# Kernel optimization log

Hardware: AMD Instinct MI355X
Metric: run time of the kernel (lower is better)

The kernel has to match this reference:

```python
import jax, jax.numpy as jnp
import numpy as np

NUMERICAL_STABILIZER = 1e-3


def relu_kernel(data, projection_matrix):
    # data: [B,L,H,D], projection_matrix: [M,D] -> [B,L,H,M]
    ratio = 1.0 / jnp.sqrt(jnp.asarray(projection_matrix.shape[0], dtype=data.dtype))
    data_dash = ratio * jnp.einsum('blhd,md->blhm', data, projection_matrix)
    return jax.nn.relu(data_dash) + NUMERICAL_STABILIZER


def favor_causal(query, key, value, projection_matrix):
    # query/key/value: [B,L,H,D]; projection_matrix: [M,D]
    qp = relu_kernel(query, projection_matrix)  # [B,L,H,M]
    kp = relu_kernel(key, projection_matrix)    # [B,L,H,M]
    # move L to scan axis: [L,B,H,*]
    qs = jnp.transpose(qp, (1, 0, 2, 3))
    ks = jnp.transpose(kp, (1, 0, 2, 3))
    vs = jnp.transpose(value, (1, 0, 2, 3))

    B, H, M = qs.shape[1], qs.shape[2], qs.shape[3]
    D = vs.shape[3]
    kv0 = jnp.zeros((B, H, M, D), dtype=qs.dtype)
    ksum0 = jnp.zeros((B, H, M), dtype=qs.dtype)

    def step(carry, inp):
        kv_sum, k_sum = carry
        q_t, k_t, v_t = inp  # [B,H,M], [B,H,M], [B,H,D]
        kv_sum = kv_sum + jnp.einsum('bhm,bhd->bhmd', k_t, v_t)
        k_sum = k_sum + k_t
        num_t = jnp.einsum('bhmd,bhm->bhd', kv_sum, q_t)  # [B,H,D]
        den_t = jnp.einsum('bhm,bhm->bh', q_t, k_sum)     # [B,H]
        return (kv_sum, k_sum), (num_t, den_t)

    _, (num, den) = jax.lax.scan(step, (kv0, ksum0), (qs, ks, vs))
    # num: [L,B,H,D], den: [L,B,H]
    out = num / den[..., None]
    return jnp.transpose(out, (1, 0, 2, 3))  # [B,L,H,D]


def setup_inputs() -> dict:
    key = jax.random.key(0)
    k1, k2, k3, k4 = jax.random.split(key, 4)
    B, L, H, D, M = 2, 4096, 8, 64, 128
    return {
        'query': jax.random.normal(k1, (B, L, H, D), dtype=jnp.float32),
        'key': jax.random.normal(k2, (B, L, H, D), dtype=jnp.float32),
        'value': jax.random.normal(k3, (B, L, H, D), dtype=jnp.float32),
        'projection_matrix': jax.random.normal(k4, (M, D), dtype=jnp.float32),
    }


def reference(query, key, value, projection_matrix):
    return favor_causal(query, key, value, projection_matrix)
```

## Files before the change

kernel.cpp:

```cpp
#include <hip/hip_runtime.h>


#define B_ 2
#define L_ 4096
#define H_ 8
#define D_ 64
#define M_ 128
#define BH_ 16
#define HD_ 512
#define LHD_ (L_*HD_)
#define EC_ (M_*D_ + M_)
#define C_ 64
#define T_ 64
#define RATIO 0.08838834764831845f
#define EPS 1e-3f

#define VT_S  72
#define KVT_S 136
#define QF_S  136
#define KF_S  136
#define SM_S  72
#define KFT_S 72

typedef __attribute__((ext_vector_type(8))) short bf16x8;
typedef __attribute__((ext_vector_type(4))) float f32x4;

__device__ __forceinline__ short f2bf(float f) {
  union { float f; unsigned u; } x; x.f = f;
  unsigned r = (x.u + 0x7fffu + ((x.u >> 16) & 1u)) >> 16;
  return (short)r;
}
__device__ __forceinline__ float bf2f(short s) {
  union { unsigned u; float f; } x; x.u = ((unsigned)(unsigned short)s) << 16;
  return x.f;
}
__device__ __forceinline__ bf16x8 load_cvt8(const float* p) {
  float4 a = *(const float4*)p;
  float4 b = *(const float4*)(p + 4);
  union { bf16x8 v; short s[8]; } u;
  u.s[0]=f2bf(a.x); u.s[1]=f2bf(a.y); u.s[2]=f2bf(a.z); u.s[3]=f2bf(a.w);
  u.s[4]=f2bf(b.x); u.s[5]=f2bf(b.y); u.s[6]=f2bf(b.z); u.s[7]=f2bf(b.w);
  return u.v;
}
#define MFMA(a,b,c) __builtin_amdgcn_mfma_f32_16x16x32_bf16((a),(b),(c),0,0,0)

__global__ __launch_bounds__(256) void p1_mfma(
    const float* __restrict__ kk, const float* __restrict__ vv,
    const float* __restrict__ P, float* __restrict__ cs)
{
  __shared__ short Vt[64*VT_S];
  __shared__ short Kft[128*KFT_S];

  const int tid = threadIdx.x;
  const int bid = blockIdx.x;
  const int bh = bid >> 6, c = bid & 63;
  const int b = bh >> 3, h = bh & 7;
  const int lane = tid & 63, w = tid >> 6, quad = lane >> 4, l15 = lane & 15;
  const size_t gbase = (size_t)b*LHD_ + (size_t)h*D_;
  float* base = cs + (size_t)(bh*C_ + c)*EC_;

  for (int fi = tid; fi < 64*16; fi += 256) {
    int t = fi >> 4, d4 = (fi & 15) * 4;
    float4 v = *(const float4*)(vv + gbase + (size_t)(c*T_ + t)*HD_ + d4);
    Vt[(d4+0)*VT_S + t] = f2bf(v.x);
    Vt[(d4+1)*VT_S + t] = f2bf(v.y);
    Vt[(d4+2)*VT_S + t] = f2bf(v.z);
    Vt[(d4+3)*VT_S + t] = f2bf(v.w);
  }

  const float* krow = kk + gbase + (size_t)(c*T_ + 16*w + l15)*HD_;
  bf16x8 ak0 = load_cvt8(krow + quad*8);
  bf16x8 ak1 = load_cvt8(krow + 32 + quad*8);
  #pragma unroll
  for (int ct = 0; ct < 8; ++ct) {
    const float* prow = P + (ct*16 + l15)*64;
    bf16x8 bp0 = load_cvt8(prow + quad*8);
    bf16x8 bp1 = load_cvt8(prow + 32 + quad*8);
    f32x4 ka = {0.f,0.f,0.f,0.f};
    ka = MFMA(ak0, bp0, ka);
    ka = MFMA(ak1, bp1, ka);
    #pragma unroll
    for (int reg = 0; reg < 4; ++reg) {
      int t = 16*w + quad*4 + reg;
      int m = l15 + 16*ct;
      Kft[m*KFT_S + t] = f2bf(fmaxf(ka[reg]*RATIO, 0.f) + EPS);
    }
  }
  __syncthreads();

  if (tid < 128) {
    float s = 0.f;
    #pragma unroll 8
    for (int t = 0; t < 64; ++t) s += bf2f(Kft[tid*KFT_S + t]);
    base[M_*D_ + tid] = s;
  }

  #pragma unroll
  for (int sb = 0; sb < 2; ++sb) {
    f32x4 acc[4];
    #pragma unroll
    for (int ct = 0; ct < 4; ++ct) { f32x4 z = {0.f,0.f,0.f,0.f}; acc[ct] = z; }
    #pragma unroll
    for (int ks2 = 0; ks2 < 2; ++ks2) {
      bf16x8 a = *(const bf16x8*)&Kft[(32*w + 16*sb + l15)*KFT_S + ks2*32 + quad*8];
      #pragma unroll
      for (int ct = 0; ct < 4; ++ct) {
        bf16x8 bb = *(const bf16x8*)&Vt[(ct*16 + l15)*VT_S + ks2*32 + quad*8];
        acc[ct] = MFMA(a, bb, acc[ct]);
      }
    }
    #pragma unroll
    for (int ct = 0; ct < 4; ++ct)
      #pragma unroll
      for (int reg = 0; reg < 4; ++reg) {
        int m = 32*w + 16*sb + quad*4 + reg;
        base[m*64 + l15 + 16*ct] = acc[ct][reg];
      }
  }
}

__global__ __launch_bounds__(256) void p2_prefix(float* __restrict__ cs)
{
  const int gid = blockIdx.x*256 + threadIdx.x;
  const int bh = gid / EC_, e = gid % EC_;
  if (bh >= BH_) return;
  float run = 0.f;
  size_t idx = (size_t)bh*C_*EC_ + e;
  for (int c = 0; c < C_; ++c, idx += EC_) {
    float tmp = cs[idx];
    cs[idx] = run;
    run += tmp;
  }
}

__global__ __launch_bounds__(256, 2) void p3_mfma(
    const float* __restrict__ qq, const float* __restrict__ kk,
    const float* __restrict__ vv, const float* __restrict__ P,
    const float* __restrict__ cs, float* __restrict__ out)
{
  __shared__ short Vt[64*VT_S];
  __shared__ short KVt[64*KVT_S];
  __shared__ short Qf[64*QF_S];
  __shared__ short Kf[64*KF_S];
  __shared__ short Sm[64*SM_S];
  __shared__ float ks[128];
  __shared__ float den2p[4][64];
  __shared__ float rowsum[64];

  const int tid = threadIdx.x;
  const int bid = blockIdx.x;
  const int bh = bid >> 6, c = bid & 63;
  const int b = bh >> 3, h = bh & 7;
  const int lane = tid & 63, w = tid >> 6, quad = lane >> 4, l15 = lane & 15;
  const size_t gbase = (size_t)b*LHD_ + (size_t)h*D_;
  const float* base = cs + (size_t)(bh*C_ + c)*EC_;

  for (int fi = tid; fi < 64*16; fi += 256) {
    int t = fi >> 4, d4 = (fi & 15) * 4;
    float4 v = *(const float4*)(vv + gbase + (size_t)(c*T_ + t)*HD_ + d4);
    Vt[(d4+0)*VT_S + t] = f2bf(v.x);
    Vt[(d4+1)*VT_S + t] = f2bf(v.y);
    Vt[(d4+2)*VT_S + t] = f2bf(v.z);
    Vt[(d4+3)*VT_S + t] = f2bf(v.w);
  }
  for (int fi = tid; fi < 128*16; fi += 256) {
    int m = fi >> 4, d4 = (fi & 15) * 4;
    float4 v = *(const float4*)(base + m*64 + d4);
    KVt[(d4+0)*KVT_S + m] = f2bf(v.x);
    KVt[(d4+1)*KVT_S + m] = f2bf(v.y);
    KVt[(d4+2)*KVT_S + m] = f2bf(v.z);
    KVt[(d4+3)*KVT_S + m] = f2bf(v.w);
  }
  if (tid < 128) ks[tid] = base[M_*D_ + tid];

  const float* qrow = qq + gbase + (size_t)(c*T_ + 16*w + l15)*HD_;
  const float* krow = kk + gbase + (size_t)(c*T_ + 16*w + l15)*HD_;
  bf16x8 aq0 = load_cvt8(qrow + quad*8);
  bf16x8 aq1 = load_cvt8(qrow + 32 + quad*8);
  bf16x8 ak0 = load_cvt8(krow + quad*8);
  bf16x8 ak1 = load_cvt8(krow + 32 + quad*8);
  #pragma unroll
  for (int ct = 0; ct < 8; ++ct) {
    const float* prow = P + (ct*16 + l15)*64;
    bf16x8 bp0 = load_cvt8(prow + quad*8);
    bf16x8 bp1 = load_cvt8(prow + 32 + quad*8);
    f32x4 qa = {0.f,0.f,0.f,0.f}, ka = {0.f,0.f,0.f,0.f};
    qa = MFMA(aq0, bp0, qa); qa = MFMA(aq1, bp1, qa);
    ka = MFMA(ak0, bp0, ka); ka = MFMA(ak1, bp1, ka);
    #pragma unroll
    for (int reg = 0; reg < 4; ++reg) {
      int row = 16*w + quad*4 + reg;
      int col = l15 + 16*ct;
      Qf[row*QF_S + col] = f2bf(fmaxf(qa[reg]*RATIO, 0.f) + EPS);
      Kf[row*KF_S + col] = f2bf(fmaxf(ka[reg]*RATIO, 0.f) + EPS);
    }
  }
  __syncthreads();

  {
    int r = tid & 63, p = tid >> 6;
    float s = 0.f;
    #pragma unroll 8
    for (int m = 32*p; m < 32*p + 32; ++m)
      s += bf2f(Qf[r*QF_S + m]) * ks[m];
    den2p[p][r] = s;
  }

  {
    f32x4 sacc[4];
    #pragma unroll
    for (int jt = 0; jt < 4; ++jt) { f32x4 z = {0.f,0.f,0.f,0.f}; sacc[jt] = z; }
    #pragma unroll
    for (int ks2 = 0; ks2 < 4; ++ks2) {
      bf16x8 a = *(const bf16x8*)&Qf[(16*w + l15)*QF_S + ks2*32 + quad*8];
      #pragma unroll
      for (int jt = 0; jt < 4; ++jt) {
        bf16x8 bb = *(const bf16x8*)&Kf[(jt*16 + l15)*KF_S + ks2*32 + quad*8];
        sacc[jt] = MFMA(a, bb, sacc[jt]);
      }
    }
    float rs[4] = {0.f,0.f,0.f,0.f};
    #pragma unroll
    for (int jt = 0; jt < 4; ++jt)
      #pragma unroll
      for (int reg = 0; reg < 4; ++reg) {
        int i = 16*w + quad*4 + reg;
        int j = l15 + 16*jt;
        float val = (j <= i) ? sacc[jt][reg] : 0.f;
        rs[reg] += val;
        Sm[i*SM_S + j] = f2bf(val);
      }
    #pragma unroll
    for (int reg = 0; reg < 4; ++reg) {
      float v = rs[reg];
      v += __shfl_xor(v, 1); v += __shfl_xor(v, 2);
      v += __shfl_xor(v, 4); v += __shfl_xor(v, 8);
      if (l15 == 0) rowsum[16*w + quad*4 + reg] = v;
    }
  }
  __syncthreads();

  f32x4 nacc[4];
  #pragma unroll
  for (int ct = 0; ct < 4; ++ct) { f32x4 z = {0.f,0.f,0.f,0.f}; nacc[ct] = z; }
  #pragma unroll
  for (int ks2 = 0; ks2 < 4; ++ks2) {
    bf16x8 a = *(const bf16x8*)&Qf[(16*w + l15)*QF_S + ks2*32 + quad*8];
    #pragma unroll
    for (int ct = 0; ct < 4; ++ct) {
      bf16x8 bb = *(const bf16x8*)&KVt[(ct*16 + l15)*KVT_S + ks2*32 + quad*8];
      nacc[ct] = MFMA(a, bb, nacc[ct]);
    }
  }
  #pragma unroll
  for (int ks2 = 0; ks2 < 2; ++ks2) {
    bf16x8 a = *(const bf16x8*)&Sm[(16*w + l15)*SM_S + ks2*32 + quad*8];
    #pragma unroll
    for (int ct = 0; ct < 4; ++ct) {
      bf16x8 bb = *(const bf16x8*)&Vt[(ct*16 + l15)*VT_S + ks2*32 + quad*8];
      nacc[ct] = MFMA(a, bb, nacc[ct]);
    }
  }

  #pragma unroll
  for (int reg = 0; reg < 4; ++reg) {
    int i = 16*w + quad*4 + reg;
    float den = den2p[0][i] + den2p[1][i] + den2p[2][i] + den2p[3][i] + rowsum[i];
    float inv = 1.f / den;
    #pragma unroll
    for (int ct = 0; ct < 4; ++ct) {
      int dcol = l15 + 16*ct;
      out[gbase + (size_t)(c*T_ + i)*HD_ + dcol] = nacc[ct][reg] * inv;
    }
  }
}

extern "C" void kernel_launch(void* const* d_in, const int* in_sizes, int n_in,
                              void* d_out, int out_size, void* d_ws, size_t ws_size,
                              hipStream_t stream) {
  const float* q = (const float*)d_in[0];
  const float* k = (const float*)d_in[1];
  const float* v = (const float*)d_in[2];
  const float* P = (const float*)d_in[3];
  float* out = (float*)d_out;
  float* cs  = (float*)d_ws;

  dim3 blk(256);
  p1_mfma  <<<dim3(BH_*C_), blk, 0, stream>>>(k, v, P, cs);
  p2_prefix<<<dim3((BH_*EC_ + 255)/256), blk, 0, stream>>>(cs);
  p3_mfma  <<<dim3(BH_*C_), blk, 0, stream>>>(q, k, v, P, cs, out);
}
```

Baseline: 154.9 us.

## Store chunk states and features in bf16 workspace, compute q/k features once

Phase 1 now computes both query and key random features and writes them as bf16 to workspace, along with per-chunk KV state stored transposed in bf16. The prefix scan works on bf16 records in groups of four, and phase 3 reads features and prefix state straight from global memory instead of recomputing projections and restaging into LDS. This halves the bytes moved for the chunk state and removes redundant projection work. In exchange, the running prefix sums are rounded to bf16 at every chunk, which costs accuracy, and phase 1 does more work and writes more data.

Result: faster. 146.3 us (-5.5%).

```diff
diff --git a/kernel.cpp b/kernel.cpp
--- a/kernel.cpp
+++ b/kernel.cpp
@@ -9,20 +9,23 @@
 #define BH_ 16
 #define HD_ 512
 #define LHD_ (L_*HD_)
-#define EC_ (M_*D_ + M_)
 #define C_ 64
 #define T_ 64
 #define RATIO 0.08838834764831845f
 #define EPS 1e-3f
 
+#define REC_CS 8320
+#define REC_F  8192
+#define CS_TOT (BH_*C_*REC_CS)
+#define QF_OFF CS_TOT
+#define KF_OFF (CS_TOT + BH_*C_*REC_F)
+
 #define VT_S  72
-#define KVT_S 136
-#define QF_S  136
-#define KF_S  136
+#define KFT_S 72
 #define SM_S  72
-#define KFT_S 72
 
 typedef __attribute__((ext_vector_type(8))) short bf16x8;
+typedef __attribute__((ext_vector_type(4))) short bf16x4;
 typedef __attribute__((ext_vector_type(4))) float f32x4;
 
 __device__ __forceinline__ short f2bf(float f) {
@@ -44,234 +47,211 @@
 }
 #define MFMA(a,b,c) __builtin_amdgcn_mfma_f32_16x16x32_bf16((a),(b),(c),0,0,0)
 
-__global__ __launch_bounds__(256) void p1_mfma(
-    const float* __restrict__ kk, const float* __restrict__ vv,
-    const float* __restrict__ P, float* __restrict__ cs)
+__global__ __launch_bounds__(256) void p1(
+    const float* __restrict__ qq, const float* __restrict__ kk,
+    const float* __restrict__ vv, const float* __restrict__ P,
+    unsigned short* __restrict__ ws)
 {
   __shared__ short Vt[64*VT_S];
   __shared__ short Kft[128*KFT_S];
 
-  const int tid = threadIdx.x;
-  const int bid = blockIdx.x;
+  const int tid = threadIdx.x, bid = blockIdx.x;
   const int bh = bid >> 6, c = bid & 63;
   const int b = bh >> 3, h = bh & 7;
   const int lane = tid & 63, w = tid >> 6, quad = lane >> 4, l15 = lane & 15;
   const size_t gbase = (size_t)b*LHD_ + (size_t)h*D_;
-  float* base = cs + (size_t)(bh*C_ + c)*EC_;
+  const int t0 = c*T_;
 
   for (int fi = tid; fi < 64*16; fi += 256) {
-    int t = fi >> 4, d4 = (fi & 15) * 4;
-    float4 v = *(const float4*)(vv + gbase + (size_t)(c*T_ + t)*HD_ + d4);
-    Vt[(d4+0)*VT_S + t] = f2bf(v.x);
-    Vt[(d4+1)*VT_S + t] = f2bf(v.y);
-    Vt[(d4+2)*VT_S + t] = f2bf(v.z);
-    Vt[(d4+3)*VT_S + t] = f2bf(v.w);
-  }
-
-  const float* krow = kk + gbase + (size_t)(c*T_ + 16*w + l15)*HD_;
-  bf16x8 ak0 = load_cvt8(krow + quad*8);
-  bf16x8 ak1 = load_cvt8(krow + 32 + quad*8);
-  #pragma unroll
-  for (int ct = 0; ct < 8; ++ct) {
-    const float* prow = P + (ct*16 + l15)*64;
-    bf16x8 bp0 = load_cvt8(prow + quad*8);
-    bf16x8 bp1 = load_cvt8(prow + 32 + quad*8);
-    f32x4 ka = {0.f,0.f,0.f,0.f};
-    ka = MFMA(ak0, bp0, ka);
-    ka = MFMA(ak1, bp1, ka);
-    #pragma unroll
-    for (int reg = 0; reg < 4; ++reg) {
-      int t = 16*w + quad*4 + reg;
-      int m = l15 + 16*ct;
-      Kft[m*KFT_S + t] = f2bf(fmaxf(ka[reg]*RATIO, 0.f) + EPS);
-    }
-  }
-  __syncthreads();
-
-  if (tid < 128) {
-    float s = 0.f;
-    #pragma unroll 8
-    for (int t = 0; t < 64; ++t) s += bf2f(Kft[tid*KFT_S + t]);
-    base[M_*D_ + tid] = s;
-  }
-
-  #pragma unroll
-  for (int sb = 0; sb < 2; ++sb) {
-    f32x4 acc[4];
-    #pragma unroll
-    for (int ct = 0; ct < 4; ++ct) { f32x4 z = {0.f,0.f,0.f,0.f}; acc[ct] = z; }
-    #pragma unroll
-    for (int ks2 = 0; ks2 < 2; ++ks2) {
-      bf16x8 a = *(const bf16x8*)&Kft[(32*w + 16*sb + l15)*KFT_S + ks2*32 + quad*8];
-      #pragma unroll
-      for (int ct = 0; ct < 4; ++ct) {
-        bf16x8 bb = *(const bf16x8*)&Vt[(ct*16 + l15)*VT_S + ks2*32 + quad*8];
-        acc[ct] = MFMA(a, bb, acc[ct]);
-      }
-    }
-    #pragma unroll
-    for (int ct = 0; ct < 4; ++ct)
-      #pragma unroll
-      for (int reg = 0; reg < 4; ++reg) {
-        int m = 32*w + 16*sb + quad*4 + reg;
-        base[m*64 + l15 + 16*ct] = acc[ct][reg];
-      }
-  }
-}
-
-__global__ __launch_bounds__(256) void p2_prefix(float* __restrict__ cs)
-{
-  const int gid = blockIdx.x*256 + threadIdx.x;
-  const int bh = gid / EC_, e = gid % EC_;
-  if (bh >= BH_) return;
-  float run = 0.f;
-  size_t idx = (size_t)bh*C_*EC_ + e;
-  for (int c = 0; c < C_; ++c, idx += EC_) {
-    float tmp = cs[idx];
-    cs[idx] = run;
-    run += tmp;
-  }
-}
-
-__global__ __launch_bounds__(256, 2) void p3_mfma(
-    const float* __restrict__ qq, const float* __restrict__ kk,
-    const float* __restrict__ vv, const float* __restrict__ P,
-    const float* __restrict__ cs, float* __restrict__ out)
-{
-  __shared__ short Vt[64*VT_S];
-  __shared__ short KVt[64*KVT_S];
-  __shared__ short Qf[64*QF_S];
-  __shared__ short Kf[64*KF_S];
-  __shared__ short Sm[64*SM_S];
-  __shared__ float ks[128];
-  __shared__ float den2p[4][64];
-  __shared__ float rowsum[64];
-
-  const int tid = threadIdx.x;
-  const int bid = blockIdx.x;
-  const int bh = bid >> 6, c = bid & 63;
-  const int b = bh >> 3, h = bh & 7;
-  const int lane = tid & 63, w = tid >> 6, quad = lane >> 4, l15 = lane & 15;
-  const size_t gbase = (size_t)b*LHD_ + (size_t)h*D_;
-  const float* base = cs + (size_t)(bh*C_ + c)*EC_;
-
-  for (int fi = tid; fi < 64*16; fi += 256) {
-    int t = fi >> 4, d4 = (fi & 15) * 4;
-    float4 v = *(const float4*)(vv + gbase + (size_t)(c*T_ + t)*HD_ + d4);
-    Vt[(d4+0)*VT_S + t] = f2bf(v.x);
-    Vt[(d4+1)*VT_S + t] = f2bf(v.y);
-    Vt[(d4+2)*VT_S + t] = f2bf(v.z);
-    Vt[(d4+3)*VT_S + t] = f2bf(v.w);
-  }
-  for (int fi = tid; fi < 128*16; fi += 256) {
-    int m = fi >> 4, d4 = (fi & 15) * 4;
-    float4 v = *(const float4*)(base + m*64 + d4);
-    KVt[(d4+0)*KVT_S + m] = f2bf(v.x);
-    KVt[(d4+1)*KVT_S + m] = f2bf(v.y);
-    KVt[(d4+2)*KVT_S + m] = f2bf(v.z);
-    KVt[(d4+3)*KVT_S + m] = f2bf(v.w);
-  }
-  if (tid < 128) ks[tid] = base[M_*D_ + tid];
-
-  const float* qrow = qq + gbase + (size_t)(c*T_ + 16*w + l15)*HD_;
-  const float* krow = kk + gbase + (size_t)(c*T_ + 16*w + l15)*HD_;
+    int t = fi >> 4, d4 = (fi & 15)*4;
+    float4 v4 = *(const float4*)(vv + gbase + (size_t)(t0+t)*HD_ + d4);
+    Vt[(d4+0)*VT_S + t] = f2bf(v4.x);
+    Vt[(d4+1)*VT_S + t] = f2bf(v4.y);
+    Vt[(d4+2)*VT_S + t] = f2bf(v4.z);
+    Vt[(d4+3)*VT_S + t] = f2bf(v4.w);
+  }
+
+  const float* qrow = qq + gbase + (size_t)(t0 + 16*w + l15)*HD_;
+  const float* krow = kk + gbase + (size_t)(t0 + 16*w + l15)*HD_;
   bf16x8 aq0 = load_cvt8(qrow + quad*8);
   bf16x8 aq1 = load_cvt8(qrow + 32 + quad*8);
   bf16x8 ak0 = load_cvt8(krow + quad*8);
   bf16x8 ak1 = load_cvt8(krow + 32 + quad*8);
+  unsigned short* qfb = ws + QF_OFF + (size_t)(bh*C_+c)*REC_F;
+  unsigned short* kfb = ws + KF_OFF + (size_t)(bh*C_+c)*REC_F;
   #pragma unroll
   for (int ct = 0; ct < 8; ++ct) {
     const float* prow = P + (ct*16 + l15)*64;
     bf16x8 bp0 = load_cvt8(prow + quad*8);
     bf16x8 bp1 = load_cvt8(prow + 32 + quad*8);
     f32x4 qa = {0.f,0.f,0.f,0.f}, ka = {0.f,0.f,0.f,0.f};
-    qa = MFMA(aq0, bp0, qa); qa = MFMA(aq1, bp1, qa);
-    ka = MFMA(ak0, bp0, ka); ka = MFMA(ak1, bp1, ka);
+    qa = MFMA(aq0,bp0,qa); qa = MFMA(aq1,bp1,qa);
+    ka = MFMA(ak0,bp0,ka); ka = MFMA(ak1,bp1,ka);
+    #pragma unroll
+    for (int reg = 0; reg < 4; ++reg) {
+      int trow = 16*w + quad*4 + reg;
+      int m = l15 + 16*ct;
+      short qv = f2bf(fmaxf(qa[reg]*RATIO, 0.f) + EPS);
+      short kv = f2bf(fmaxf(ka[reg]*RATIO, 0.f) + EPS);
+      qfb[trow*128 + m] = (unsigned short)qv;
+      kfb[trow*128 + m] = (unsigned short)kv;
+      Kft[m*KFT_S + trow] = kv;
+    }
+  }
+  __syncthreads();
+
+  unsigned short* csb = ws + (size_t)(bh*C_+c)*REC_CS;
+  bf16x8 av0 = *(const bf16x8*)&Vt[(16*w + l15)*VT_S + quad*8];
+  bf16x8 av1 = *(const bf16x8*)&Vt[(16*w + l15)*VT_S + 32 + quad*8];
+  #pragma unroll
+  for (int mt = 0; mt < 8; ++mt) {
+    f32x4 acc = {0.f,0.f,0.f,0.f};
+    bf16x8 b0 = *(const bf16x8*)&Kft[(16*mt + l15)*KFT_S + quad*8];
+    bf16x8 b1 = *(const bf16x8*)&Kft[(16*mt + l15)*KFT_S + 32 + quad*8];
+    acc = MFMA(av0, b0, acc);
+    acc = MFMA(av1, b1, acc);
+    #pragma unroll
+    for (int reg = 0; reg < 4; ++reg) {
+      int d = 16*w + quad*4 + reg;
+      int m = l15 + 16*mt;
+      csb[d*128 + m] = (unsigned short)f2bf(acc[reg]);
+    }
+  }
+  if (tid < 128) {
+    float s = 0.f;
+    #pragma unroll 8
+    for (int t = 0; t < 64; ++t) s += bf2f(Kft[tid*KFT_S + t]);
+    csb[64*128 + tid] = (unsigned short)f2bf(s);
+  }
+}
+
+__global__ __launch_bounds__(256) void p2(unsigned short* __restrict__ ws)
+{
+  const int gid = blockIdx.x*256 + threadIdx.x;
+  if (gid >= BH_*(REC_CS/4)) return;
+  const int bh = gid / (REC_CS/4), g = gid % (REC_CS/4);
+  unsigned short* base = ws + (size_t)bh*C_*REC_CS + g*4;
+  float run[4] = {0.f,0.f,0.f,0.f};
+  #pragma unroll 1
+  for (int c = 0; c < C_; c += 4) {
+    bf16x4 r[4];
+    #pragma unroll
+    for (int u = 0; u < 4; ++u)
+      r[u] = *(const bf16x4*)(base + (size_t)(c+u)*REC_CS);
+    #pragma unroll
+    for (int u = 0; u < 4; ++u) {
+      union { bf16x4 v; short s[4]; } wv;
+      #pragma unroll
+      for (int j = 0; j < 4; ++j) { wv.s[j] = f2bf(run[j]); run[j] += bf2f(r[u][j]); }
+      *(bf16x4*)(base + (size_t)(c+u)*REC_CS) = wv.v;
+    }
+  }
+}
+
+__global__ __launch_bounds__(256) void p3(
+    const float* __restrict__ vv, const unsigned short* __restrict__ ws,
+    float* __restrict__ out)
+{
+  __shared__ short Vt[64*VT_S];
+  __shared__ short Sm[64*SM_S];
+  __shared__ float ks_lds[128];
+
+  const int tid = threadIdx.x, bid = blockIdx.x;
+  const int bh = bid >> 6, c = bid & 63;
+  const int b = bh >> 3, h = bh & 7;
+  const int lane = tid & 63, w = tid >> 6, quad = lane >> 4, l15 = lane & 15;
+  const size_t gbase = (size_t)b*LHD_ + (size_t)h*D_;
+  const int t0 = c*T_;
+  const unsigned short* csb = ws + (size_t)(bh*C_+c)*REC_CS;
+  const unsigned short* qfb = ws + QF_OFF + (size_t)(bh*C_+c)*REC_F;
+  const unsigned short* kfb = ws + KF_OFF + (size_t)(bh*C_+c)*REC_F;
+
+  for (int fi = tid; fi < 64*16; fi += 256) {
+    int t = fi >> 4, d4 = (fi & 15)*4;
+    float4 v4 = *(const float4*)(vv + gbase + (size_t)(t0+t)*HD_ + d4);
+    Vt[(d4+0)*VT_S + t] = f2bf(v4.x);
+    Vt[(d4+1)*VT_S + t] = f2bf(v4.y);
+    Vt[(d4+2)*VT_S + t] = f2bf(v4.z);
+    Vt[(d4+3)*VT_S + t] = f2bf(v4.w);
+  }
+  if (tid < 128) ks_lds[tid] = bf2f((short)csb[64*128 + tid]);
+
+  bf16x8 qf[4];
+  #pragma unroll
+  for (int ks2 = 0; ks2 < 4; ++ks2)
+    qf[ks2] = *(const bf16x8*)(qfb + (16*w + l15)*128 + ks2*32 + quad*8);
+
+  __syncthreads();
+
+  f32x4 nacc[4];
+  #pragma unroll
+  for (int ct = 0; ct < 4; ++ct) { f32x4 z = {0.f,0.f,0.f,0.f}; nacc[ct] = z; }
+  #pragma unroll
+  for (int ks2 = 0; ks2 < 4; ++ks2) {
+    #pragma unroll
+    for (int ct = 0; ct < 4; ++ct) {
+      bf16x8 bb = *(const bf16x8*)(csb + (16*ct + l15)*128 + ks2*32 + quad*8);
+      nacc[ct] = MFMA(qf[ks2], bb, nacc[ct]);
+    }
+  }
+
+  float dp = 0.f;
+  #pragma unroll
+  for (int ks2 = 0; ks2 < 4; ++ks2)
+    #pragma unroll
+    for (int j = 0; j < 8; ++j)
+      dp += bf2f(qf[ks2][j]) * ks_lds[ks2*32 + quad*8 + j];
+  dp += __shfl_xor(dp, 16);
+  dp += __shfl_xor(dp, 32);
+
+  f32x4 sacc[4];
+  #pragma unroll
+  for (int jt = 0; jt < 4; ++jt) { f32x4 z = {0.f,0.f,0.f,0.f}; sacc[jt] = z; }
+  #pragma unroll
+  for (int ks2 = 0; ks2 < 4; ++ks2) {
+    #pragma unroll
+    for (int jt = 0; jt < 4; ++jt) {
+      bf16x8 bb = *(const bf16x8*)(kfb + (16*jt + l15)*128 + ks2*32 + quad*8);
+      sacc[jt] = MFMA(qf[ks2], bb, sacc[jt]);
+    }
+  }
+  float rs[4] = {0.f,0.f,0.f,0.f};
+  #pragma unroll
+  for (int jt = 0; jt < 4; ++jt)
     #pragma unroll
     for (int reg = 0; reg < 4; ++reg) {
       int row = 16*w + quad*4 + reg;
-      int col = l15 + 16*ct;
-      Qf[row*QF_S + col] = f2bf(fmaxf(qa[reg]*RATIO, 0.f) + EPS);
-      Kf[row*KF_S + col] = f2bf(fmaxf(ka[reg]*RATIO, 0.f) + EPS);
-    }
-  }
-  __syncthreads();
-
-  {
-    int r = tid & 63, p = tid >> 6;
-    float s = 0.f;
-    #pragma unroll 8
-    for (int m = 32*p; m < 32*p + 32; ++m)
-      s += bf2f(Qf[r*QF_S + m]) * ks[m];
-    den2p[p][r] = s;
-  }
-
-  {
-    f32x4 sacc[4];
-    #pragma unroll
-    for (int jt = 0; jt < 4; ++jt) { f32x4 z = {0.f,0.f,0.f,0.f}; sacc[jt] = z; }
-    #pragma unroll
-    for (int ks2 = 0; ks2 < 4; ++ks2) {
-      bf16x8 a = *(const bf16x8*)&Qf[(16*w + l15)*QF_S + ks2*32 + quad*8];
-      #pragma unroll
-      for (int jt = 0; jt < 4; ++jt) {
-        bf16x8 bb = *(const bf16x8*)&Kf[(jt*16 + l15)*KF_S + ks2*32 + quad*8];
-        sacc[jt] = MFMA(a, bb, sacc[jt]);
-      }
-    }
-    float rs[4] = {0.f,0.f,0.f,0.f};
-    #pragma unroll
-    for (int jt = 0; jt < 4; ++jt)
-      #pragma unroll
-      for (int reg = 0; reg < 4; ++reg) {
-        int i = 16*w + quad*4 + reg;
-        int j = l15 + 16*jt;
-        float val = (j <= i) ? sacc[jt][reg] : 0.f;
-        rs[reg] += val;
-        Sm[i*SM_S + j] = f2bf(val);
-      }
-    #pragma unroll
-    for (int reg = 0; reg < 4; ++reg) {
-      float v = rs[reg];
-      v += __shfl_xor(v, 1); v += __shfl_xor(v, 2);
-      v += __shfl_xor(v, 4); v += __shfl_xor(v, 8);
-      if (l15 == 0) rowsum[16*w + quad*4 + reg] = v;
-    }
-  }
-  __syncthreads();
-
-  f32x4 nacc[4];
-  #pragma unroll
-  for (int ct = 0; ct < 4; ++ct) { f32x4 z = {0.f,0.f,0.f,0.f}; nacc[ct] = z; }
-  #pragma unroll
-  for (int ks2 = 0; ks2 < 4; ++ks2) {
-    bf16x8 a = *(const bf16x8*)&Qf[(16*w + l15)*QF_S + ks2*32 + quad*8];
+      int j = l15 + 16*jt;
+      float val = (j <= row) ? sacc[jt][reg] : 0.f;
+      rs[reg] += val;
+      Sm[row*SM_S + j] = f2bf(val);
+    }
+  #pragma unroll
+  for (int reg = 0; reg < 4; ++reg) {
+    rs[reg] += __shfl_xor(rs[reg], 1);
+    rs[reg] += __shfl_xor(rs[reg], 2);
+    rs[reg] += __shfl_xor(rs[reg], 4);
+    rs[reg] += __shfl_xor(rs[reg], 8);
+  }
+
+  #pragma unroll
+  for (int ks = 0; ks < 2; ++ks) {
+    bf16x8 a = *(const bf16x8*)&Sm[(16*w + l15)*SM_S + ks*32 + quad*8];
     #pragma unroll
     for (int ct = 0; ct < 4; ++ct) {
-      bf16x8 bb = *(const bf16x8*)&KVt[(ct*16 + l15)*KVT_S + ks2*32 + quad*8];
+      bf16x8 bb = *(const bf16x8*)&Vt[(16*ct + l15)*VT_S + ks*32 + quad*8];
       nacc[ct] = MFMA(a, bb, nacc[ct]);
     }
   }
-  #pragma unroll
-  for (int ks2 = 0; ks2 < 2; ++ks2) {
-    bf16x8 a = *(const bf16x8*)&Sm[(16*w + l15)*SM_S + ks2*32 + quad*8];
-    #pragma unroll
-    for (int ct = 0; ct < 4; ++ct) {
-      bf16x8 bb = *(const bf16x8*)&Vt[(ct*16 + l15)*VT_S + ks2*32 + quad*8];
-      nacc[ct] = MFMA(a, bb, nacc[ct]);
-    }
-  }
 
   #pragma unroll
   for (int reg = 0; reg < 4; ++reg) {
-    int i = 16*w + quad*4 + reg;
-    float den = den2p[0][i] + den2p[1][i] + den2p[2][i] + den2p[3][i] + rowsum[i];
-    float inv = 1.f / den;
-    #pragma unroll
-    for (int ct = 0; ct < 4; ++ct) {
-      int dcol = l15 + 16*ct;
-      out[gbase + (size_t)(c*T_ + i)*HD_ + dcol] = nacc[ct][reg] * inv;
-    }
+    float den1 = __shfl(dp, 4*quad + reg);
+    float inv = 1.f / (den1 + rs[reg]);
+    int trow = t0 + 16*w + quad*4 + reg;
+    #pragma unroll
+    for (int ct = 0; ct < 4; ++ct)
+      out[gbase + (size_t)trow*HD_ + 16*ct + l15] = nacc[ct][reg] * inv;
   }
 }
 
@@ -283,10 +263,10 @@
   const float* v = (const float*)d_in[2];
   const float* P = (const float*)d_in[3];
   float* out = (float*)d_out;
-  float* cs  = (float*)d_ws;
+  unsigned short* ws = (unsigned short*)d_ws;
 
   dim3 blk(256);
-  p1_mfma  <<<dim3(BH_*C_), blk, 0, stream>>>(k, v, P, cs);
-  p2_prefix<<<dim3((BH_*EC_ + 255)/256), blk, 0, stream>>>(cs);
-  p3_mfma  <<<dim3(BH_*C_), blk, 0, stream>>>(q, k, v, P, cs, out);
-}
+  p1<<<dim3(BH_*C_), blk, 0, stream>>>(q, k, v, P, ws);
+  p2<<<dim3((BH_*(REC_CS/4) + 255)/256), blk, 0, stream>>>(ws);
+  p3<<<dim3(BH_*C_), blk, 0, stream>>>(v, ws, out);
+}
```
